# Kernel tuning notes

Hardware: AMD Instinct MI355X
Metric: run time of the kernel (lower is better)

## Reference

```python
import jax, jax.numpy as jnp
import numpy as np

B, NPER, F, D, E, NUM_STEPS = 256, 512, 256, 32, 524288, 4
N = B * NPER
INIT_TAU, TAU_SCALE, STEP_ALPHA = 0.1, 0.5, 5.0


def setup_inputs() -> dict:
    key = jax.random.key(0)
    ks = jax.random.split(key, 10)
    x_start = jax.random.uniform(ks[0], (N,), jnp.float32, 0.1, 1.0)   # strictly positive iterate
    x_solution = jax.random.uniform(ks[1], (N,), jnp.float32, 0.0, 1.0)
    q = jax.random.normal(ks[2], (N,), jnp.float32)
    edge_src = jax.random.randint(ks[3], (E,), 0, N, jnp.int32)
    edge_dst = jax.random.randint(ks[4], (E,), 0, N, jnp.int32)
    vals_batch = jnp.repeat(jnp.arange(B, dtype=jnp.int32), NPER)      # equal-sized graphs
    proj_matrix = jax.random.normal(ks[5], (B, NPER, F), jnp.float32) / np.float32(np.sqrt(NPER))
    W_in = jax.random.normal(ks[6], (2, D), jnp.float32) / np.float32(np.sqrt(2.0))
    b_in = jnp.zeros((D,), jnp.float32)
    W_msg = jax.random.normal(ks[7], (D, D), jnp.float32) / np.float32(np.sqrt(D))
    b_msg = jnp.zeros((D,), jnp.float32)
    W_out = jax.random.normal(ks[8], (D, 1), jnp.float32) / np.float32(np.sqrt(D))
    b_out = jnp.zeros((1,), jnp.float32)
    return {"x_start": x_start, "x_solution": x_solution, "q": q,
            "proj_matrix": proj_matrix, "W_in": W_in, "b_in": b_in,
            "W_msg": W_msg, "b_msg": b_msg, "W_out": W_out, "b_out": b_out,
            "edge_src": edge_src, "edge_dst": edge_dst, "vals_batch": vals_batch}


def _l1_normalize(x, batch):
    # per-graph L1 normalization: x / sum_i |x_i| over the graph segment
    s = jax.ops.segment_sum(jnp.abs(x), batch, num_segments=B)
    return x / (s[batch] + 1e-12)


def _line_search(x, d, batch, max_alpha):
    # largest per-graph alpha s.t. x + alpha*d >= 0, capped at max_alpha
    ratio = jnp.where(d < 0, x / jnp.maximum(-d, 1e-12), max_alpha)
    a = jnp.clip(jax.ops.segment_min(ratio, batch, num_segments=B), 0.0, max_alpha)
    return a[batch]  # gathered back to per-node


def _gnn(xs, q, edge_src, edge_dst, W_in, b_in, W_msg, b_msg, W_out, b_out):
    h = jax.nn.relu(jnp.stack([xs, q], axis=-1) @ W_in + b_in)      # [N, D]
    m = h[edge_src] @ W_msg + b_msg                                  # [E, D]
    agg = jax.ops.segment_sum(m, edge_dst, num_segments=N)          # [N, D]
    h2 = jax.nn.relu(h + agg)
    return h2 @ W_out[:, 0] + b_out[0]                               # [N]


def reference(x_start, x_solution, q, proj_matrix, W_in, b_in, W_msg, b_msg,
              W_out, b_out, edge_src, edge_dst, vals_batch):
    tau = INIT_TAU
    xs = x_start
    preds, labels = [], []
    for _ in range(NUM_STEPS):
        pred = _gnn(xs, q, edge_src, edge_dst, W_in, b_in, W_msg, b_msg, W_out, b_out)
        preds.append(pred)
        labels.append(_l1_normalize(x_solution - xs, vals_batch))
        p = _l1_normalize(jax.lax.stop_gradient(pred), vals_batch)   # .detach() in torch
        direction = p + 3.0 * tau / (xs + tau)
        tau = max(tau * TAU_SCALE, 1e-5)
        # to_dense_batch with equal graph sizes == reshape; project onto nullspace basis
        dd = direction.reshape(B, NPER)
        df = jnp.einsum('bnf,bn->bf', proj_matrix, dd)               # [B, F]
        pproj = jnp.einsum('bnf,bf->bn', proj_matrix, df).reshape(-1)  # [N]
        alpha = _line_search(xs, pproj, vals_batch, STEP_ALPHA) * 0.995
        xs = xs + alpha * pproj
    return jnp.stack(preds, axis=1), jnp.stack(labels, axis=1)       # each [N, NUM_STEPS]
```

## Files before the change

kernel.cpp:

```cpp
#include <hip/hip_runtime.h>

#define BB 256
#define NPER 512
#define FF 256
#define DD 32
#define EE 524288
#define NN (BB*NPER)
#define NSTEPS 4

__device__ __forceinline__ float bflo(unsigned u) { return __uint_as_float(u << 16); }
__device__ __forceinline__ float bfhi(unsigned u) { return __uint_as_float(u & 0xFFFF0000u); }


__global__ void k_deg(const int* __restrict__ dst, unsigned* __restrict__ deg) {
    int e = blockIdx.x * blockDim.x + threadIdx.x;
    atomicAdd(&deg[dst[e]], 1u);
}

__global__ void k_bsum(const unsigned* __restrict__ deg, unsigned* __restrict__ bsum) {
    __shared__ unsigned r[256];
    int t = threadIdx.x;
    r[t] = deg[blockIdx.x * 256 + t];
    __syncthreads();
    for (int o = 128; o > 0; o >>= 1) { if (t < o) r[t] += r[t + o]; __syncthreads(); }
    if (t == 0) bsum[blockIdx.x] = r[0];
}

__global__ void k_scanb(const unsigned* __restrict__ bsum, unsigned* __restrict__ bbase) {
    __shared__ unsigned r[512];
    int t = threadIdx.x;
    unsigned own = bsum[t];
    r[t] = own;
    __syncthreads();
    for (int o = 1; o < 512; o <<= 1) {
        unsigned v = (t >= o) ? r[t - o] : 0u;
        __syncthreads();
        r[t] += v;
        __syncthreads();
    }
    bbase[t] = r[t] - own;
}

__global__ void k_offsets(const unsigned* __restrict__ deg, const unsigned* __restrict__ bbase,
                          unsigned* __restrict__ rowstart, unsigned* __restrict__ cursor) {
    __shared__ unsigned r[256];
    int t = threadIdx.x;
    int i = blockIdx.x * 256 + t;
    unsigned d = deg[i];
    r[t] = d;
    __syncthreads();
    for (int o = 1; o < 256; o <<= 1) {
        unsigned v = (t >= o) ? r[t - o] : 0u;
        __syncthreads();
        r[t] += v;
        __syncthreads();
    }
    unsigned excl = r[t] - d + bbase[blockIdx.x];
    rowstart[i] = excl;
    cursor[i] = excl;
}

__global__ void k_fill(const int* __restrict__ src, const int* __restrict__ dst,
                       unsigned* __restrict__ cursor, int* __restrict__ csr_src) {
    int e = blockIdx.x * blockDim.x + threadIdx.x;
    unsigned pos = atomicAdd(&cursor[dst[e]], 1u);
    csr_src[pos] = src[e];
}

__global__ void k_cast(const float* __restrict__ P, unsigned* __restrict__ Pbf2) {
    size_t i = (size_t)(blockIdx.x * blockDim.x + threadIdx.x);
    float4 p = ((const float4*)P)[i];
    unsigned u0 = __float_as_uint(p.x), u1 = __float_as_uint(p.y);
    unsigned u2 = __float_as_uint(p.z), u3 = __float_as_uint(p.w);
    u0 = (u0 + 0x7FFFu + ((u0 >> 16) & 1u)) >> 16;
    u1 = (u1 + 0x7FFFu + ((u1 >> 16) & 1u)) >> 16;
    u2 = (u2 + 0x7FFFu + ((u2 >> 16) & 1u)) >> 16;
    u3 = (u3 + 0x7FFFu + ((u3 >> 16) & 1u)) >> 16;
    uint2 o; o.x = u0 | (u1 << 16); o.y = u2 | (u3 << 16);
    ((uint2*)Pbf2)[i] = o;
}


__global__ void k_node_g(const float* __restrict__ xs, const float* __restrict__ q,
                         const float* __restrict__ Win, const float* __restrict__ bin,
                         const unsigned* __restrict__ rowstart, const unsigned* __restrict__ deg,
                         const int* __restrict__ csr_src,
                         const float* __restrict__ Wmsg, const float* __restrict__ bmsg,
                         const float* __restrict__ Wout, const float* __restrict__ bout,
                         float* __restrict__ pred, float* __restrict__ out_preds, int step) {
    __shared__ float Wm[DD * DD];
    __shared__ float sl[8 * DD];
    int tid = threadIdx.x;
    int ni = tid >> 5, d = tid & 31;
    int i = blockIdx.x * 8 + ni;
    for (int k = tid; k < DD * DD; k += 256) Wm[k] = Wmsg[k];
    float w0 = Win[d], w1 = Win[DD + d], b0 = bin[d];
    unsigned rs = rowstart[i];
    unsigned dg = deg[i];
    unsigned nfull = dg < 32u ? dg : 32u;
    float xv = 0.f, qv = 0.f;
    if ((unsigned)d < nfull) {
        int sv = csr_src[rs + d];
        xv = xs[sv]; qv = q[sv];
    }
    float s = 0.f;
    for (unsigned j = 0; j < nfull; ++j) {
        float xj = __shfl(xv, (int)j, 32);
        float qj = __shfl(qv, (int)j, 32);
        s += fmaxf(xj * w0 + qj * w1 + b0, 0.f);
    }
    for (unsigned j = 32; j < dg; ++j) {
        int sv = csr_src[rs + j];
        s += fmaxf(xs[sv] * w0 + q[sv] * w1 + b0, 0.f);
    }
    sl[tid] = s;
    __syncthreads();
    float hval = fmaxf(xs[i] * w0 + q[i] * w1 + b0, 0.f);
    float agg = (float)dg * bmsg[d];
    const float* srow = &sl[ni * DD];
    #pragma unroll
    for (int k = 0; k < DD; ++k) agg += srow[k] * Wm[k * DD + d];
    float h2 = fmaxf(hval + agg, 0.f);
    float v = h2 * Wout[d];
    for (int o = 16; o > 0; o >>= 1) v += __shfl_down(v, o, 32);
    if (d == 0) {
        float pr = v + bout[0];
        pred[i] = pr;
        out_preds[i * NSTEPS + step] = pr;
    }
}

__global__ void k_graph(const float* __restrict__ xs, const float* __restrict__ xsol,
                        const float* __restrict__ pred,
                        float* __restrict__ out_labels, float* __restrict__ dd,
                        unsigned int* __restrict__ alphaMin, float tau, int step) {
    __shared__ float s1[8], s2[8];
    int b = blockIdx.x;
    int t = threadIdx.x;
    int wid = t >> 6;
    int lane = t & 63;
    int i = b * NPER + t;
    float x = xs[i];
    float r = xsol[i] - x;
    float p = pred[i];
    float a1 = fabsf(r), a2 = fabsf(p);
    #pragma unroll
    for (int o = 32; o > 0; o >>= 1) {
        a1 += __shfl_down(a1, o, 64);
        a2 += __shfl_down(a2, o, 64);
    }
    if (lane == 0) { s1[wid] = a1; s2[wid] = a2; }
    __syncthreads();
    float Sr = 1e-12f, Sp = 1e-12f;
    #pragma unroll
    for (int k = 0; k < 8; ++k) { Sr += s1[k]; Sp += s2[k]; }
    out_labels[i * NSTEPS + step] = r / Sr;
    dd[i] = p / Sp + 3.0f * tau / (x + tau);
    if (t == 0) alphaMin[b] = 0x7f800000u;
}

__global__ void k_df(const unsigned short* __restrict__ Pbf, const float* __restrict__ dd,
                     float* __restrict__ dfp) {
    __shared__ float dl[128];
    __shared__ float sl[4 * FF];
    int b = blockIdx.x >> 2, sp = blockIdx.x & 3;
    int t = threadIdx.x, w = t >> 6, lane = t & 63;
    if (t < 128) dl[t] = dd[b * NPER + sp * 128 + t];
    __syncthreads();
    const uint2* P2 = (const uint2*)(Pbf + (size_t)(b * NPER + sp * 128 + w * 32) * FF) + lane;
    float4 acc = {0.f, 0.f, 0.f, 0.f};
    const float* dw = &dl[w * 32];
    #pragma unroll 4
    for (int n = 0; n < 32; ++n) {
        uint2 pv = P2[(size_t)n * 64];
        float sc = dw[n];
        acc.x += bflo(pv.x) * sc; acc.y += bfhi(pv.x) * sc;
        acc.z += bflo(pv.y) * sc; acc.w += bfhi(pv.y) * sc;
    }
    ((float4*)sl)[w * 64 + lane] = acc;
    __syncthreads();
    float v = sl[t] + sl[FF + t] + sl[2 * FF + t] + sl[3 * FF + t];
    dfp[((b << 2) + sp) * FF + t] = v;
}

__global__ void k_pproj(const unsigned short* __restrict__ Pbf, const float* __restrict__ dfp,
                        const float* __restrict__ xs,
                        float* __restrict__ pproj, unsigned int* __restrict__ alphaMin) {
    __shared__ float mred[4];
    int t = threadIdx.x, w = t >> 6, lane = t & 63;
    int n0 = blockIdx.x * 16 + w * 4;
    int b = blockIdx.x >> 5;
    const float4* dp = (const float4*)dfp + (size_t)(b << 2) * 64 + lane;
    float4 d0 = dp[0], d1 = dp[64], d2 = dp[128], d3 = dp[192];
    float4 df4 = {d0.x + d1.x + d2.x + d3.x, d0.y + d1.y + d2.y + d3.y,
                  d0.z + d1.z + d2.z + d3.z, d0.w + d1.w + d2.w + d3.w};
    const uint2* P2 = (const uint2*)(Pbf + (size_t)n0 * FF) + lane;
    uint2 p0 = P2[0], p1 = P2[64], p2 = P2[128], p3 = P2[192];
    float a0 = bflo(p0.x) * df4.x + bfhi(p0.x) * df4.y + bflo(p0.y) * df4.z + bfhi(p0.y) * df4.w;
    float a1 = bflo(p1.x) * df4.x + bfhi(p1.x) * df4.y + bflo(p1.y) * df4.z + bfhi(p1.y) * df4.w;
    float a2 = bflo(p2.x) * df4.x + bfhi(p2.x) * df4.y + bflo(p2.y) * df4.z + bfhi(p2.y) * df4.w;
    float a3 = bflo(p3.x) * df4.x + bfhi(p3.x) * df4.y + bflo(p3.y) * df4.z + bfhi(p3.y) * df4.w;
    #pragma unroll
    for (int o = 32; o > 0; o >>= 1) {
        a0 += __shfl_down(a0, o, 64);
        a1 += __shfl_down(a1, o, 64);
        a2 += __shfl_down(a2, o, 64);
        a3 += __shfl_down(a3, o, 64);
    }
    if (lane == 0) {
        float acc[4] = {a0, a1, a2, a3};
        float m = 5.0f;
        #pragma unroll
        for (int k = 0; k < 4; ++k) {
            pproj[n0 + k] = acc[k];
            float x = xs[n0 + k];
            float ratio = (acc[k] < 0.f) ? (x / fmaxf(-acc[k], 1e-12f)) : 5.0f;
            m = fminf(m, ratio);
        }
        mred[w] = m;
    }
    __syncthreads();
    if (t == 0) {
        float m = fminf(fminf(mred[0], mred[1]), fminf(mred[2], mred[3]));
        atomicMin(&alphaMin[b], __float_as_uint(m));
    }
}

__global__ void k_update(const unsigned int* __restrict__ alphaMin,
                         const float* __restrict__ pproj, float* __restrict__ xs) {
    int i = blockIdx.x * blockDim.x + threadIdx.x;
    int b = i >> 9;
    float a = __uint_as_float(alphaMin[b]);
    a = fminf(fmaxf(a, 0.f), 5.0f) * 0.995f;
    xs[i] += a * pproj[i];
}


extern "C" void kernel_launch(void* const* d_in, const int* in_sizes, int n_in,
                              void* d_out, int out_size, void* d_ws, size_t ws_size,
                              hipStream_t stream) {
    const float* x_start = (const float*)d_in[0];
    const float* x_sol   = (const float*)d_in[1];
    const float* q       = (const float*)d_in[2];
    const float* P       = (const float*)d_in[3];
    const float* Win     = (const float*)d_in[4];
    const float* bin     = (const float*)d_in[5];
    const float* Wmsg    = (const float*)d_in[6];
    const float* bmsg    = (const float*)d_in[7];
    const float* Wout    = (const float*)d_in[8];
    const float* bout    = (const float*)d_in[9];
    const int*   esrc    = (const int*)d_in[10];
    const int*   edst    = (const int*)d_in[11];

    float* out_preds  = (float*)d_out;
    float* out_labels = (float*)d_out + (size_t)NN * NSTEPS;

    float* w = (float*)d_ws;
    float* xs    = w; w += NN;
    float* pred  = w; w += NN;
    float* ddv   = w; w += NN;
    float* pproj = w; w += NN;
    float* dfp   = w; w += (size_t)BB * 4 * FF;
    unsigned* alphaMin = (unsigned*)w; w += BB;
    unsigned* deg      = (unsigned*)w; w += NN;
    unsigned* rowstart = (unsigned*)w; w += NN;
    unsigned* cursor   = (unsigned*)w; w += NN;
    unsigned* bsum     = (unsigned*)w; w += NN / 256;
    unsigned* bbase    = (unsigned*)w; w += NN / 256;
    int* csr_src       = (int*)w;      w += EE;
    unsigned short* Pbf = (unsigned short*)w;

    hipMemsetAsync(deg, 0, NN * sizeof(unsigned), stream);
    k_deg<<<EE / 256, 256, 0, stream>>>(edst, deg);
    k_cast<<<(BB * NPER * FF / 4) / 256, 256, 0, stream>>>(P, (unsigned*)Pbf);
    k_bsum<<<NN / 256, 256, 0, stream>>>(deg, bsum);
    k_scanb<<<1, NN / 256, 0, stream>>>(bsum, bbase);
    k_offsets<<<NN / 256, 256, 0, stream>>>(deg, bbase, rowstart, cursor);
    k_fill<<<EE / 256, 256, 0, stream>>>(esrc, edst, cursor, csr_src);

    hipMemcpyAsync(xs, x_start, NN * sizeof(float), hipMemcpyDeviceToDevice, stream);

    float tau = 0.1f;
    for (int step = 0; step < NSTEPS; ++step) {
        k_node_g<<<NN / 8, 256, 0, stream>>>(xs, q, Win, bin, rowstart, deg, csr_src,
                                             Wmsg, bmsg, Wout, bout, pred, out_preds, step);
        k_graph<<<BB, NPER, 0, stream>>>(xs, x_sol, pred, out_labels, ddv, alphaMin,
                                         tau, step);
        if (step < NSTEPS - 1) {
            k_df<<<BB * 4, 256, 0, stream>>>(Pbf, ddv, dfp);
            k_pproj<<<NN / 16, 256, 0, stream>>>(Pbf, dfp, xs, pproj, alphaMin);
            k_update<<<NN / 256, 256, 0, stream>>>(alphaMin, pproj, xs);
        }
        tau = fmaxf(tau * 0.5f, 1e-5f);
    }
}
```

Before: 548.3 us.

## Pack xs/q into float2, shuffle-based GNN matvec, atomic df reduction, retile pproj

Packs xs and q into one interleaved float2 array so each neighbour gather in the GNN kernel is a single 8-byte load instead of two scattered loads. The message matvec now keeps the W_msg column in registers and broadcasts partial sums with shuffles, removing shared memory and a block barrier. The per-graph df partials are combined with atomicAdd into one zeroed buffer instead of four partial copies. The projection kernel is retiled so half-waves do 16-byte loads covering 8 nodes per wave. This adds a pack kernel and float atomics, which makes the summation order nondeterministic.

New measurement: 525.3 us. -4.2%, faster.

```diff
diff --git a/kernel.cpp b/kernel.cpp
--- a/kernel.cpp
+++ b/kernel.cpp
@@ -80,28 +80,36 @@
     ((uint2*)Pbf2)[i] = o;
 }
 
-
-__global__ void k_node_g(const float* __restrict__ xs, const float* __restrict__ q,
+__global__ void k_pack(const float* __restrict__ xs0, const float* __restrict__ q,
+                       float2* __restrict__ xq) {
+    int i = blockIdx.x * blockDim.x + threadIdx.x;
+    float2 v; v.x = xs0[i]; v.y = q[i];
+    xq[i] = v;
+}
+
+
+__global__ void k_node_g(const float2* __restrict__ xq,
                          const float* __restrict__ Win, const float* __restrict__ bin,
                          const unsigned* __restrict__ rowstart, const unsigned* __restrict__ deg,
                          const int* __restrict__ csr_src,
                          const float* __restrict__ Wmsg, const float* __restrict__ bmsg,
                          const float* __restrict__ Wout, const float* __restrict__ bout,
                          float* __restrict__ pred, float* __restrict__ out_preds, int step) {
-    __shared__ float Wm[DD * DD];
-    __shared__ float sl[8 * DD];
     int tid = threadIdx.x;
-    int ni = tid >> 5, d = tid & 31;
-    int i = blockIdx.x * 8 + ni;
-    for (int k = tid; k < DD * DD; k += 256) Wm[k] = Wmsg[k];
+    int d = tid & 31;
+    int i = blockIdx.x * 8 + (tid >> 5);
     float w0 = Win[d], w1 = Win[DD + d], b0 = bin[d];
+    float wcol[DD];
+    #pragma unroll
+    for (int k = 0; k < DD; ++k) wcol[k] = Wmsg[k * DD + d];
     unsigned rs = rowstart[i];
     unsigned dg = deg[i];
     unsigned nfull = dg < 32u ? dg : 32u;
     float xv = 0.f, qv = 0.f;
     if ((unsigned)d < nfull) {
         int sv = csr_src[rs + d];
-        xv = xs[sv]; qv = q[sv];
+        float2 v = xq[sv];
+        xv = v.x; qv = v.y;
     }
     float s = 0.f;
     for (unsigned j = 0; j < nfull; ++j) {
@@ -111,15 +119,14 @@
     }
     for (unsigned j = 32; j < dg; ++j) {
         int sv = csr_src[rs + j];
-        s += fmaxf(xs[sv] * w0 + q[sv] * w1 + b0, 0.f);
-    }
-    sl[tid] = s;
-    __syncthreads();
-    float hval = fmaxf(xs[i] * w0 + q[i] * w1 + b0, 0.f);
+        float2 v = xq[sv];
+        s += fmaxf(v.x * w0 + v.y * w1 + b0, 0.f);
+    }
+    float2 self = xq[i];
+    float hval = fmaxf(self.x * w0 + self.y * w1 + b0, 0.f);
     float agg = (float)dg * bmsg[d];
-    const float* srow = &sl[ni * DD];
-    #pragma unroll
-    for (int k = 0; k < DD; ++k) agg += srow[k] * Wm[k * DD + d];
+    #pragma unroll
+    for (int k = 0; k < DD; ++k) agg += __shfl(s, k, 32) * wcol[k];
     float h2 = fmaxf(hval + agg, 0.f);
     float v = h2 * Wout[d];
     for (int o = 16; o > 0; o >>= 1) v += __shfl_down(v, o, 32);
@@ -130,9 +137,10 @@
     }
 }
 
-__global__ void k_graph(const float* __restrict__ xs, const float* __restrict__ xsol,
+__global__ void k_graph(const float2* __restrict__ xq, const float* __restrict__ xsol,
                         const float* __restrict__ pred,
                         float* __restrict__ out_labels, float* __restrict__ dd,
+                        float* __restrict__ df,
                         unsigned int* __restrict__ alphaMin, float tau, int step) {
     __shared__ float s1[8], s2[8];
     int b = blockIdx.x;
@@ -140,7 +148,7 @@
     int wid = t >> 6;
     int lane = t & 63;
     int i = b * NPER + t;
-    float x = xs[i];
+    float x = xq[i].x;
     float r = xsol[i] - x;
     float p = pred[i];
     float a1 = fabsf(r), a2 = fabsf(p);
@@ -156,11 +164,12 @@
     for (int k = 0; k < 8; ++k) { Sr += s1[k]; Sp += s2[k]; }
     out_labels[i * NSTEPS + step] = r / Sr;
     dd[i] = p / Sp + 3.0f * tau / (x + tau);
+    if (t < FF) df[b * FF + t] = 0.f;
     if (t == 0) alphaMin[b] = 0x7f800000u;
 }
 
 __global__ void k_df(const unsigned short* __restrict__ Pbf, const float* __restrict__ dd,
-                     float* __restrict__ dfp) {
+                     float* __restrict__ df) {
     __shared__ float dl[128];
     __shared__ float sl[4 * FF];
     int b = blockIdx.x >> 2, sp = blockIdx.x & 3;
@@ -180,59 +189,53 @@
     ((float4*)sl)[w * 64 + lane] = acc;
     __syncthreads();
     float v = sl[t] + sl[FF + t] + sl[2 * FF + t] + sl[3 * FF + t];
-    dfp[((b << 2) + sp) * FF + t] = v;
-}
-
-__global__ void k_pproj(const unsigned short* __restrict__ Pbf, const float* __restrict__ dfp,
-                        const float* __restrict__ xs,
+    atomicAdd(&df[b * FF + t], v);
+}
+
+__global__ void k_pproj(const unsigned short* __restrict__ Pbf, const float* __restrict__ df,
+                        const float2* __restrict__ xq,
                         float* __restrict__ pproj, unsigned int* __restrict__ alphaMin) {
     __shared__ float mred[4];
     int t = threadIdx.x, w = t >> 6, lane = t & 63;
-    int n0 = blockIdx.x * 16 + w * 4;
-    int b = blockIdx.x >> 5;
-    const float4* dp = (const float4*)dfp + (size_t)(b << 2) * 64 + lane;
-    float4 d0 = dp[0], d1 = dp[64], d2 = dp[128], d3 = dp[192];
-    float4 df4 = {d0.x + d1.x + d2.x + d3.x, d0.y + d1.y + d2.y + d3.y,
-                  d0.z + d1.z + d2.z + d3.z, d0.w + d1.w + d2.w + d3.w};
-    const uint2* P2 = (const uint2*)(Pbf + (size_t)n0 * FF) + lane;
-    uint2 p0 = P2[0], p1 = P2[64], p2 = P2[128], p3 = P2[192];
-    float a0 = bflo(p0.x) * df4.x + bfhi(p0.x) * df4.y + bflo(p0.y) * df4.z + bfhi(p0.y) * df4.w;
-    float a1 = bflo(p1.x) * df4.x + bfhi(p1.x) * df4.y + bflo(p1.y) * df4.z + bfhi(p1.y) * df4.w;
-    float a2 = bflo(p2.x) * df4.x + bfhi(p2.x) * df4.y + bflo(p2.y) * df4.z + bfhi(p2.y) * df4.w;
-    float a3 = bflo(p3.x) * df4.x + bfhi(p3.x) * df4.y + bflo(p3.y) * df4.z + bfhi(p3.y) * df4.w;
-    #pragma unroll
-    for (int o = 32; o > 0; o >>= 1) {
-        a0 += __shfl_down(a0, o, 64);
-        a1 += __shfl_down(a1, o, 64);
-        a2 += __shfl_down(a2, o, 64);
-        a3 += __shfl_down(a3, o, 64);
-    }
-    if (lane == 0) {
-        float acc[4] = {a0, a1, a2, a3};
-        float m = 5.0f;
+    int hl = lane >> 5, l5 = lane & 31;
+    int b = blockIdx.x >> 4;
+    const float4* dfp4 = (const float4*)(df + (size_t)b * FF);
+    float4 dfa = dfp4[l5 * 2], dfb = dfp4[l5 * 2 + 1];
+    int n0 = blockIdx.x * 32 + w * 8 + hl;
+    float m = 5.0f;
+    #pragma unroll
+    for (int it = 0; it < 4; ++it) {
+        int n = n0 + it * 2;
+        uint4 pv = ((const uint4*)(Pbf + (size_t)n * FF))[l5];
+        float acc = bflo(pv.x) * dfa.x + bfhi(pv.x) * dfa.y
+                  + bflo(pv.y) * dfa.z + bfhi(pv.y) * dfa.w
+                  + bflo(pv.z) * dfb.x + bfhi(pv.z) * dfb.y
+                  + bflo(pv.w) * dfb.z + bfhi(pv.w) * dfb.w;
         #pragma unroll
-        for (int k = 0; k < 4; ++k) {
-            pproj[n0 + k] = acc[k];
-            float x = xs[n0 + k];
-            float ratio = (acc[k] < 0.f) ? (x / fmaxf(-acc[k], 1e-12f)) : 5.0f;
+        for (int o = 16; o > 0; o >>= 1) acc += __shfl_down(acc, o, 32);
+        if (l5 == 0) {
+            pproj[n] = acc;
+            float x = xq[n].x;
+            float ratio = (acc < 0.f) ? (x / fmaxf(-acc, 1e-12f)) : 5.0f;
             m = fminf(m, ratio);
         }
-        mred[w] = m;
-    }
+    }
+    m = fminf(m, __shfl_xor(m, 32, 64));
+    if (lane == 0) mred[w] = m;
     __syncthreads();
     if (t == 0) {
-        float m = fminf(fminf(mred[0], mred[1]), fminf(mred[2], mred[3]));
-        atomicMin(&alphaMin[b], __float_as_uint(m));
+        float mm = fminf(fminf(mred[0], mred[1]), fminf(mred[2], mred[3]));
+        atomicMin(&alphaMin[b], __float_as_uint(mm));
     }
 }
 
 __global__ void k_update(const unsigned int* __restrict__ alphaMin,
-                         const float* __restrict__ pproj, float* __restrict__ xs) {
+                         const float* __restrict__ pproj, float2* __restrict__ xq) {
     int i = blockIdx.x * blockDim.x + threadIdx.x;
     int b = i >> 9;
     float a = __uint_as_float(alphaMin[b]);
     a = fminf(fmaxf(a, 0.f), 5.0f) * 0.995f;
-    xs[i] += a * pproj[i];
+    xq[i].x += a * pproj[i];
 }
 
 
@@ -256,11 +259,11 @@
     float* out_labels = (float*)d_out + (size_t)NN * NSTEPS;
 
     float* w = (float*)d_ws;
-    float* xs    = w; w += NN;
+    float2* xq  = (float2*)w; w += 2 * (size_t)NN;
     float* pred  = w; w += NN;
     float* ddv   = w; w += NN;
     float* pproj = w; w += NN;
-    float* dfp   = w; w += (size_t)BB * 4 * FF;
+    float* df    = w; w += (size_t)BB * FF;
     unsigned* alphaMin = (unsigned*)w; w += BB;
     unsigned* deg      = (unsigned*)w; w += NN;
     unsigned* rowstart = (unsigned*)w; w += NN;
@@ -273,23 +276,22 @@
     hipMemsetAsync(deg, 0, NN * sizeof(unsigned), stream);
     k_deg<<<EE / 256, 256, 0, stream>>>(edst, deg);
     k_cast<<<(BB * NPER * FF / 4) / 256, 256, 0, stream>>>(P, (unsigned*)Pbf);
+    k_pack<<<NN / 256, 256, 0, stream>>>(x_start, q, xq);
     k_bsum<<<NN / 256, 256, 0, stream>>>(deg, bsum);
     k_scanb<<<1, NN / 256, 0, stream>>>(bsum, bbase);
     k_offsets<<<NN / 256, 256, 0, stream>>>(deg, bbase, rowstart, cursor);
     k_fill<<<EE / 256, 256, 0, stream>>>(esrc, edst, cursor, csr_src);
 
-    hipMemcpyAsync(xs, x_start, NN * sizeof(float), hipMemcpyDeviceToDevice, stream);
-
     float tau = 0.1f;
     for (int step = 0; step < NSTEPS; ++step) {
-        k_node_g<<<NN / 8, 256, 0, stream>>>(xs, q, Win, bin, rowstart, deg, csr_src,
+        k_node_g<<<NN / 8, 256, 0, stream>>>(xq, Win, bin, rowstart, deg, csr_src,
                                              Wmsg, bmsg, Wout, bout, pred, out_preds, step);
-        k_graph<<<BB, NPER, 0, stream>>>(xs, x_sol, pred, out_labels, ddv, alphaMin,
+        k_graph<<<BB, NPER, 0, stream>>>(xq, x_sol, pred, out_labels, ddv, df, alphaMin,
                                          tau, step);
         if (step < NSTEPS - 1) {
-            k_df<<<BB * 4, 256, 0, stream>>>(Pbf, ddv, dfp);
-            k_pproj<<<NN / 16, 256, 0, stream>>>(Pbf, dfp, xs, pproj, alphaMin);
-            k_update<<<NN / 256, 256, 0, stream>>>(alphaMin, pproj, xs);
+            k_df<<<BB * 4, 256, 0, stream>>>(Pbf, ddv, df);
+            k_pproj<<<NN / 32, 256, 0, stream>>>(Pbf, df, xq, pproj, alphaMin);
+            k_update<<<NN / 256, 256, 0, stream>>>(alphaMin, pproj, xq);
         }
         tau = fmaxf(tau * 0.5f, 1e-5f);
     }
```
